# Optimization experiments

Hardware: AMD Instinct MI355X
Metric: run time of the kernel (lower is better)

Reference implementation:

```python
import jax, jax.numpy as jnp
import numpy as np

NCLASSES = 1000
K = 5
REG_STRENGTH = 1.0


def isotonic_l2(y):
    """Solve min_v 0.5||v - y||^2 s.t. v_1 >= v_2 >= ... >= v_n, per row.

    Uses the exact min-max characterization of isotonic regression:
      sol_i = min_{j<=i} max_{k>=i} mean(y[j..k])
    (equivalent to pool-adjacent-violators), fully vectorized.
    y: [B, n] -> [B, n]
    """
    b, n = y.shape
    cs = jnp.concatenate([jnp.zeros((b, 1), y.dtype), jnp.cumsum(y, axis=-1)], axis=-1)  # [B, n+1]
    j = jnp.arange(n)[:, None]  # block start
    k = jnp.arange(n)[None, :]  # block end
    length = (k - j + 1).astype(y.dtype)
    # M[b, j, k] = mean(y[b, j..k]) for k >= j, else -inf (ignored by the max)
    M = (cs[:, None, 1:] - cs[:, :-1, None]) / jnp.where(k >= j, length, 1.0)
    M = jnp.where(k >= j, M, -jnp.inf)
    A = jax.lax.cummax(M, axis=2, reverse=True)  # A[b, j, i] = max_{k>=i} M[b, j, k]
    A = jnp.where(j <= k, A, jnp.inf)            # restrict min to j <= i
    return jnp.min(A, axis=1)                     # [B, n]


def soft_rank(values, strength):
    """torchsort.soft_rank with l2 regularization.

    r = theta - sigma^{-1}(isotonic_l2(sort_desc(theta) - w)),  theta = values/strength,
    w = [n, n-1, ..., 1].  Larger values get larger (soft) ranks.
    """
    n = values.shape[-1]
    theta = values / strength
    perm = jnp.argsort(-theta, axis=-1)                 # descending order
    s = jnp.take_along_axis(theta, perm, axis=-1)
    inv_perm = jnp.argsort(perm, axis=-1)
    w = jnp.arange(n, 0, -1, dtype=values.dtype)
    sol = isotonic_l2(s - w[None, :])
    return jnp.take_along_axis(s - sol, inv_perm, axis=-1)


def setup_inputs() -> dict:
    key = jax.random.key(0)
    k1, k2 = jax.random.split(key)
    output = jax.random.normal(k1, (64, NCLASSES), dtype=jnp.float32)
    target = jax.random.randint(k2, (64,), 0, NCLASSES, dtype=jnp.int32)
    return {"output": output, "target": target}


def reference(output, target):
    ranks = soft_rank(output, REG_STRENGTH)                              # [B, n]
    ranks_label = jnp.take_along_axis(ranks, target[:, None], axis=-1)   # [B, 1]
    return jnp.mean(jax.nn.relu(NCLASSES - ranks_label - K + 1))
```

## Files before the change

kernel.cpp:

```cpp
#include <hip/hip_runtime.h>
#include <math.h>

#define N      1000
#define NTH1   512
#define NTH2   256
#define MSLICE 16
#define SROW   1008
#define META   (64 * SROW)

__device__ inline unsigned fkey(float x) {
    unsigned u = __float_as_uint(x);
    return (u & 0x80000000u) ? ~u : (u | 0x80000000u);
}
__device__ inline float fdecode(unsigned u) {
    return __uint_as_float((u & 0x80000000u) ? (u & 0x7FFFFFFFu) : ~u);
}

__global__ __launch_bounds__(NTH1) void k1_sort_scan(
    const float* __restrict__ mat, const int* __restrict__ target,
    float* __restrict__ ws)
{
    __shared__ float sx[2][1024];
    __shared__ float wtot[8];
    __shared__ int   cnt_sh;

    const int tid  = threadIdx.x;
    const int lane = tid & 63;
    const int w    = tid >> 6;
    const int i0   = (w << 7) + lane;
    const int i1   = i0 + 64;
    const int r    = blockIdx.x;
    const float* row = mat + r * N;
    const int   tgt  = target[r];
    const float tval = row[tgt];

    float r0 = row[i0];
    float r1 = (i1 < N) ? row[i1] : -INFINITY;
    if (tid == 0) cnt_sh = 0;

    int lc = ((r0 > tval) || (r0 == tval && i0 < tgt))
           + ((r1 > tval) || (r1 == tval && i1 < tgt));
    #pragma unroll
    for (int off = 32; off; off >>= 1) lc += __shfl_down(lc, off);
    __syncthreads();
    if (lane == 0 && lc) atomicAdd(&cnt_sh, lc);

    auto cas_shfl = [&](float& rr, int i, unsigned k, unsigned j) {
        float o = __shfl_xor(rr, (int)j);
        bool lower = ((lane & (int)j) == 0);
        bool desc  = ((i & (int)k) == 0);
        rr = (lower == desc) ? fmaxf(rr, o) : fminf(rr, o);
    };
    #pragma unroll
    for (unsigned k = 2; k <= 64; k <<= 1)
        #pragma unroll
        for (unsigned j = k >> 1; j; j >>= 1) { cas_shfl(r0, i0, k, j); cas_shfl(r1, i1, k, j); }
    int buf = 0;
    #pragma unroll
    for (unsigned k = 128; k <= 1024; k <<= 1) {
        #pragma unroll
        for (unsigned j = k >> 1; j >= 128; j >>= 1) {
            sx[buf][i0] = r0; sx[buf][i1] = r1;
            __syncthreads();
            float o0 = sx[buf][i0 ^ (int)j], o1 = sx[buf][i1 ^ (int)j];
            buf ^= 1;
            bool lower = ((i0 & (int)j) == 0);
            bool desc  = ((i0 & (int)k) == 0);
            r0 = (lower == desc) ? fmaxf(r0, o0) : fminf(r0, o0);
            r1 = (lower == desc) ? fmaxf(r1, o1) : fminf(r1, o1);
        }
        {
            bool desc = ((i0 & (int)k) == 0);
            float a = fmaxf(r0, r1), b = fminf(r0, r1);
            r0 = desc ? a : b;
            r1 = desc ? b : a;
        }
        #pragma unroll
        for (unsigned j = 32; j; j >>= 1) { cas_shfl(r0, i0, k, j); cas_shfl(r1, i1, k, j); }
    }

    if (i1 >= N) r1 = 0.0f;
    float incl0 = r0;
    #pragma unroll
    for (int off = 1; off < 64; off <<= 1) {
        float y = __shfl_up(incl0, off);
        if (lane >= off) incl0 += y;
    }
    float tot0 = __shfl(incl0, 63);
    float incl1 = r1;
    #pragma unroll
    for (int off = 1; off < 64; off <<= 1) {
        float y = __shfl_up(incl1, off);
        if (lane >= off) incl1 += y;
    }
    if (lane == 63) wtot[w] = incl0 + incl1;
    __syncthreads();
    float base = 0.0f;
    #pragma unroll
    for (int u = 0; u < 8; ++u) { float t = wtot[u]; if (u < w) base += t; }

    float* Sg = ws + r * SROW;
    if (tid == 0) Sg[0] = 0.0f;
    Sg[i0 + 1] = base + incl0;
    if (i1 < N) Sg[i1 + 1] = base + tot0 + incl1;
    if (tid == 0) {
        ((int*)ws)[META + r]            = cnt_sh;
        ws[META + 64 + r]               = tval;
        ((unsigned*)ws)[META + 128 + r] = 0xFFFFFFFFu;
    }
}

__global__ __launch_bounds__(NTH2) void k2_minmax(
    const float* __restrict__ ws, unsigned* __restrict__ mr)
{
    __shared__ float Sloc[N];
    __shared__ float rtab[N];
    __shared__ float maxh[NTH2];

    const int r  = blockIdx.y;
    const int m  = blockIdx.x;
    const int t  = threadIdx.x;
    const int p  = ((const int*)ws)[META + r];
    const int j0 = m * 64;
    if (j0 > p) return;
    const int len = N - p;
    const float* Srow = ws + r * SROW;

    const int jl = t & 63;
    const int j  = j0 + jl;
    const float Sj = (j <= p) ? Srow[j] : 0.0f;

    for (int i = t; i < len; i += NTH2) Sloc[i] = Srow[p + 1 + i];
    for (int d = t; d < N; d += NTH2) rtab[d] = 1.0f / (float)(d + 1);
    __syncthreads();

    const int q  = t >> 6;
    const int k0 = (q * len) >> 2;
    const int k1 = ((q + 1) * len) >> 2;
    float maxv = -INFINITY;
    if (j <= p) {
        const float* sp = &Sloc[k0];
        const float* rp = &rtab[p + k0 - j];
        float c = 0.5f * (float)(j + p + k0) - (float)N;
        #pragma unroll 8
        for (int it = 0; it < k1 - k0; ++it) {
            float mval = fmaf(sp[it] - Sj, rp[it], c);
            maxv = fmaxf(maxv, mval);
            c += 0.5f;
        }
    }
    maxh[t] = maxv;
    __syncthreads();
    if (t < 64) {
        float mv = fmaxf(fmaxf(maxh[t], maxh[t + 64]),
                         fmaxf(maxh[t + 128], maxh[t + 192]));
        float minv = (j0 + t <= p) ? mv : INFINITY;
        #pragma unroll
        for (int off = 32; off; off >>= 1)
            minv = fminf(minv, __shfl_down(minv, off));
        if (t == 0) atomicMin(&mr[r], fkey(minv));
    }
}

__global__ __launch_bounds__(64) void k3_loss(
    const unsigned* __restrict__ mr, const float* __restrict__ tv,
    float* __restrict__ out, int nrows)
{
    int t = threadIdx.x;
    float loss = 0.0f;
    if (t < nrows) {
        float sol  = fdecode(mr[t]);
        float rank = tv[t] - sol;
        loss = fmaxf(0.0f, (float)(N - 5 + 1) - rank);
    }
    #pragma unroll
    for (int off = 32; off; off >>= 1) loss += __shfl_down(loss, off);
    if (t == 0) out[0] = loss / (float)nrows;
}

__global__ __launch_bounds__(NTH1) void topk_loss_mono(
    const float* __restrict__ mat, const int* __restrict__ target,
    float* __restrict__ d_out, int nrows)
{
    __shared__ float S[1025];
    __shared__ float rcp[N];
    __shared__ float sx[1024];
    __shared__ float wtot[8];
    __shared__ float red[8];
    __shared__ int   cnt_sh;

    const int tid  = threadIdx.x;
    const int lane = tid & 63;
    const int w    = tid >> 6;
    const int i0   = (w << 7) + lane;
    const int i1   = i0 + 64;
    const float* row = mat + blockIdx.x * N;
    const int   tgt  = target[blockIdx.x];
    const float tval = row[tgt];

    float r0 = row[i0];
    float r1 = (i1 < N) ? row[i1] : -INFINITY;
    if (tid == 0) cnt_sh = 0;
    rcp[tid] = 1.0f / (float)(tid + 1);
    if (tid + NTH1 < N) rcp[tid + NTH1] = 1.0f / (float)(tid + NTH1 + 1);

    int lc = ((r0 > tval) || (r0 == tval && i0 < tgt))
           + ((r1 > tval) || (r1 == tval && i1 < tgt));
    #pragma unroll
    for (int off = 32; off; off >>= 1) lc += __shfl_down(lc, off);
    __syncthreads();
    if (lane == 0 && lc) atomicAdd(&cnt_sh, lc);

    auto cas_shfl = [&](float& rr, int i, unsigned k, unsigned j) {
        float o = __shfl_xor(rr, (int)j);
        bool lower = ((lane & (int)j) == 0);
        bool desc  = ((i & (int)k) == 0);
        rr = (lower == desc) ? fmaxf(rr, o) : fminf(rr, o);
    };
    #pragma unroll
    for (unsigned k = 2; k <= 64; k <<= 1)
        #pragma unroll
        for (unsigned j = k >> 1; j; j >>= 1) { cas_shfl(r0, i0, k, j); cas_shfl(r1, i1, k, j); }
    #pragma unroll
    for (unsigned k = 128; k <= 1024; k <<= 1) {
        #pragma unroll
        for (unsigned j = k >> 1; j >= 128; j >>= 1) {
            __syncthreads();
            sx[i0] = r0; sx[i1] = r1;
            __syncthreads();
            float o0 = sx[i0 ^ (int)j], o1 = sx[i1 ^ (int)j];
            bool lower = ((i0 & (int)j) == 0);
            bool desc  = ((i0 & (int)k) == 0);
            r0 = (lower == desc) ? fmaxf(r0, o0) : fminf(r0, o0);
            r1 = (lower == desc) ? fmaxf(r1, o1) : fminf(r1, o1);
        }
        {
            bool desc = ((i0 & (int)k) == 0);
            float a = fmaxf(r0, r1), b = fminf(r0, r1);
            r0 = desc ? a : b;
            r1 = desc ? b : a;
        }
        #pragma unroll
        for (unsigned j = 32; j; j >>= 1) { cas_shfl(r0, i0, k, j); cas_shfl(r1, i1, k, j); }
    }

    if (i1 >= N) r1 = 0.0f;
    float incl0 = r0;
    #pragma unroll
    for (int off = 1; off < 64; off <<= 1) {
        float y = __shfl_up(incl0, off);
        if (lane >= off) incl0 += y;
    }
    float tot0 = __shfl(incl0, 63);
    float incl1 = r1;
    #pragma unroll
    for (int off = 1; off < 64; off <<= 1) {
        float y = __shfl_up(incl1, off);
        if (lane >= off) incl1 += y;
    }
    if (lane == 63) wtot[w] = incl0 + incl1;
    __syncthreads();
    float base = 0.0f;
    #pragma unroll
    for (int u = 0; u < 8; ++u) { float t = wtot[u]; if (u < w) base += t; }
    if (tid == 0) S[0] = 0.0f;
    S[i0 + 1] = base + incl0;
    S[i1 + 1] = base + tot0 + incl1;
    __syncthreads();

    const int p   = cnt_sh;
    const int len = N - p;
    float minv = INFINITY;
    for (int j = tid; j <= p; j += NTH1) {
        const float  Sj = S[j];
        const float* Sp = &S[p + 1];
        const float* rp = &rcp[p - j];
        const float  cj = 0.5f * (float)(j + p) - (float)N;
        float maxv = -INFINITY;
        #pragma unroll 8
        for (int it = 0; it < len; ++it) {
            float mm = fmaf(Sp[it] - Sj, rp[it], cj + 0.5f * (float)it);
            maxv = fmaxf(maxv, mm);
        }
        minv = fminf(minv, maxv);
    }
    #pragma unroll
    for (int off = 32; off; off >>= 1) minv = fminf(minv, __shfl_down(minv, off));
    if (lane == 0) red[w] = minv;
    __syncthreads();
    if (tid == 0) {
        float sol = red[0];
        #pragma unroll
        for (int u = 1; u < 8; ++u) sol = fminf(sol, red[u]);
        float rank_label = tval - sol;
        float loss = fmaxf(0.0f, (float)(N - 5 + 1) - rank_label);
        atomicAdd(d_out, loss / (float)nrows);
    }
}

extern "C" void kernel_launch(void* const* d_in, const int* in_sizes, int n_in,
                              void* d_out, int out_size, void* d_ws, size_t ws_size,
                              hipStream_t stream) {
    (void)n_in;
    const float* mat    = (const float*)d_in[0];
    const int*   target = (const int*)d_in[1];
    float*       out    = (float*)d_out;
    const int    nrows  = in_sizes[1];

    const size_t need = (size_t)(META + 256) * sizeof(float);
    if (nrows == 64 && ws_size >= need) {
        float*    ws = (float*)d_ws;
        int*      pw = (int*)(ws + META);        (void)pw;
        float*    tv = ws + META + 64;
        unsigned* mr = (unsigned*)(ws + META + 128);
        k1_sort_scan<<<nrows, NTH1, 0, stream>>>(mat, target, ws);
        dim3 g2(MSLICE, nrows);
        k2_minmax<<<g2, NTH2, 0, stream>>>(ws, mr);
        k3_loss<<<1, 64, 0, stream>>>(mr, tv, out, nrows);
    } else {
        hipMemsetAsync(out, 0, sizeof(float) * out_size, stream);
        topk_loss_mono<<<nrows, NTH1, 0, stream>>>(mat, target, out, nrows);
    }
}
```

Measured before the change: 69.34 us.

## Fuse sort-scan and min-max stages into one kernel per row

Merges the sort/prefix-scan kernel and the sliced min-max kernel into a single per-row block that keeps the prefix sums in shared memory and computes the per-row loss directly. This drops the global workspace round trip, the atomicMin encoding and one kernel launch. In exchange, each row's min-max work now runs on one 512-thread block instead of 16 blocks of 256 threads, which lowers parallelism from up to 1024 blocks to 64 and uses more shared memory per block.

Result: slower. 72.77 us (+4.9%).

```diff
diff --git a/kernel.cpp b/kernel.cpp
--- a/kernel.cpp
+++ b/kernel.cpp
@@ -2,26 +2,19 @@
 #include <math.h>
 
 #define N      1000
+#define K      5
 #define NTH1   512
-#define NTH2   256
-#define MSLICE 16
-#define SROW   1008
-#define META   (64 * SROW)
-
-__device__ inline unsigned fkey(float x) {
-    unsigned u = __float_as_uint(x);
-    return (u & 0x80000000u) ? ~u : (u | 0x80000000u);
-}
-__device__ inline float fdecode(unsigned u) {
-    return __uint_as_float((u & 0x80000000u) ? (u & 0x7FFFFFFFu) : ~u);
-}
-
-__global__ __launch_bounds__(NTH1) void k1_sort_scan(
+
+__global__ __launch_bounds__(NTH1) void k1_fused(
     const float* __restrict__ mat, const int* __restrict__ target,
-    float* __restrict__ ws)
+    float* __restrict__ lossw)
 {
     __shared__ float sx[2][1024];
+    __shared__ float S[1025];
+    __shared__ float rtab[N];
+    __shared__ float pm[8][16][64];
     __shared__ float wtot[8];
+    __shared__ float redm[8];
     __shared__ int   cnt_sh;
 
     const int tid  = threadIdx.x;
@@ -37,6 +30,8 @@
     float r0 = row[i0];
     float r1 = (i1 < N) ? row[i1] : -INFINITY;
     if (tid == 0) cnt_sh = 0;
+    rtab[tid] = 1.0f / (float)(tid + 1);
+    if (tid + NTH1 < N) rtab[tid + NTH1] = 1.0f / (float)(tid + NTH1 + 1);
 
     int lc = ((r0 > tval) || (r0 == tval && i0 < tgt))
            + ((r1 > tval) || (r1 == tval && i1 < tgt));
@@ -99,80 +94,60 @@
     #pragma unroll
     for (int u = 0; u < 8; ++u) { float t = wtot[u]; if (u < w) base += t; }
 
-    float* Sg = ws + r * SROW;
-    if (tid == 0) Sg[0] = 0.0f;
-    Sg[i0 + 1] = base + incl0;
-    if (i1 < N) Sg[i1 + 1] = base + tot0 + incl1;
+    if (tid == 0) S[0] = 0.0f;
+    S[i0 + 1] = base + incl0;
+    if (i1 < N) S[i1 + 1] = base + tot0 + incl1;
+    __syncthreads();
+
+    const int p   = cnt_sh;
+    const int len = N - p;
+    const int k0q = (w * len) >> 3;
+    const int k1q = ((w + 1) * len) >> 3;
+    const float* sp = &S[p + 1 + k0q];
+    float pmax[16];
+    #pragma unroll
+    for (int jb = 0; jb < 16; ++jb) {
+        float mv = -INFINITY;
+        const int j = (jb << 6) + lane;
+        if ((jb << 6) <= p && j <= p) {
+            const float  Sj = S[j];
+            const float* rp = &rtab[p + k0q - j];
+            float c = 0.5f * (float)(j + p + k0q) - (float)N;
+            #pragma unroll 8
+            for (int it = 0; it < k1q - k0q; ++it) {
+                mv = fmaxf(mv, fmaf(sp[it] - Sj, rp[it], c));
+                c += 0.5f;
+            }
+        }
+        pm[w][jb][lane] = mv;
+    }
+    __syncthreads();
+
+    auto comb = [&](int jb) -> float {
+        float m = pm[0][jb][lane];
+        #pragma unroll
+        for (int o = 1; o < 8; ++o) m = fmaxf(m, pm[o][jb][lane]);
+        return (((jb << 6) + lane) <= p) ? m : INFINITY;
+    };
+    float minv = fminf(comb(w), comb(8 + w));
+    #pragma unroll
+    for (int off = 32; off; off >>= 1) minv = fminf(minv, __shfl_down(minv, off));
+    if (lane == 0) redm[w] = minv;
+    __syncthreads();
     if (tid == 0) {
-        ((int*)ws)[META + r]            = cnt_sh;
-        ws[META + 64 + r]               = tval;
-        ((unsigned*)ws)[META + 128 + r] = 0xFFFFFFFFu;
-    }
-}
-
-__global__ __launch_bounds__(NTH2) void k2_minmax(
-    const float* __restrict__ ws, unsigned* __restrict__ mr)
-{
-    __shared__ float Sloc[N];
-    __shared__ float rtab[N];
-    __shared__ float maxh[NTH2];
-
-    const int r  = blockIdx.y;
-    const int m  = blockIdx.x;
-    const int t  = threadIdx.x;
-    const int p  = ((const int*)ws)[META + r];
-    const int j0 = m * 64;
-    if (j0 > p) return;
-    const int len = N - p;
-    const float* Srow = ws + r * SROW;
-
-    const int jl = t & 63;
-    const int j  = j0 + jl;
-    const float Sj = (j <= p) ? Srow[j] : 0.0f;
-
-    for (int i = t; i < len; i += NTH2) Sloc[i] = Srow[p + 1 + i];
-    for (int d = t; d < N; d += NTH2) rtab[d] = 1.0f / (float)(d + 1);
-    __syncthreads();
-
-    const int q  = t >> 6;
-    const int k0 = (q * len) >> 2;
-    const int k1 = ((q + 1) * len) >> 2;
-    float maxv = -INFINITY;
-    if (j <= p) {
-        const float* sp = &Sloc[k0];
-        const float* rp = &rtab[p + k0 - j];
-        float c = 0.5f * (float)(j + p + k0) - (float)N;
-        #pragma unroll 8
-        for (int it = 0; it < k1 - k0; ++it) {
-            float mval = fmaf(sp[it] - Sj, rp[it], c);
-            maxv = fmaxf(maxv, mval);
-            c += 0.5f;
-        }
-    }
-    maxh[t] = maxv;
-    __syncthreads();
-    if (t < 64) {
-        float mv = fmaxf(fmaxf(maxh[t], maxh[t + 64]),
-                         fmaxf(maxh[t + 128], maxh[t + 192]));
-        float minv = (j0 + t <= p) ? mv : INFINITY;
-        #pragma unroll
-        for (int off = 32; off; off >>= 1)
-            minv = fminf(minv, __shfl_down(minv, off));
-        if (t == 0) atomicMin(&mr[r], fkey(minv));
+        float sol = redm[0];
+        #pragma unroll
+        for (int u = 1; u < 8; ++u) sol = fminf(sol, redm[u]);
+        float rank = tval - sol;
+        lossw[r] = fmaxf(0.0f, (float)(N - K + 1) - rank);
     }
 }
 
 __global__ __launch_bounds__(64) void k3_loss(
-    const unsigned* __restrict__ mr, const float* __restrict__ tv,
-    float* __restrict__ out, int nrows)
+    const float* __restrict__ lossw, float* __restrict__ out, int nrows)
 {
     int t = threadIdx.x;
-    float loss = 0.0f;
-    if (t < nrows) {
-        float sol  = fdecode(mr[t]);
-        float rank = tv[t] - sol;
-        loss = fmaxf(0.0f, (float)(N - 5 + 1) - rank);
-    }
+    float loss = (t < nrows) ? lossw[t] : 0.0f;
     #pragma unroll
     for (int off = 32; off; off >>= 1) loss += __shfl_down(loss, off);
     if (t == 0) out[0] = loss / (float)nrows;
@@ -307,16 +282,10 @@
     float*       out    = (float*)d_out;
     const int    nrows  = in_sizes[1];
 
-    const size_t need = (size_t)(META + 256) * sizeof(float);
-    if (nrows == 64 && ws_size >= need) {
-        float*    ws = (float*)d_ws;
-        int*      pw = (int*)(ws + META);        (void)pw;
-        float*    tv = ws + META + 64;
-        unsigned* mr = (unsigned*)(ws + META + 128);
-        k1_sort_scan<<<nrows, NTH1, 0, stream>>>(mat, target, ws);
-        dim3 g2(MSLICE, nrows);
-        k2_minmax<<<g2, NTH2, 0, stream>>>(ws, mr);
-        k3_loss<<<1, 64, 0, stream>>>(mr, tv, out, nrows);
+    if (nrows == 64 && ws_size >= 64 * sizeof(float)) {
+        float* lossw = (float*)d_ws;
+        k1_fused<<<nrows, NTH1, 0, stream>>>(mat, target, lossw);
+        k3_loss<<<1, 64, 0, stream>>>(lossw, out, nrows);
     } else {
         hipMemsetAsync(out, 0, sizeof(float) * out_size, stream);
         topk_loss_mono<<<nrows, NTH1, 0, stream>>>(mat, target, out, nrows);
```
